# Performance work log

Hardware: AMD Instinct MI355X
Metric: run time of the kernel (lower is better)

## Reference

```python
import jax, jax.numpy as jnp
import numpy as np

D = 256; H = 4; DK = D // H
MAX_ATOMS = 13; EDGE_NUM = 78; PAD = 799; K = 20
PREFIX = MAX_ATOMS * 2 + 2 + EDGE_NUM * 4   # 340, tokens that get positional encoding
SEQ = PREFIX + K                             # 360
NPAIR = EDGE_NUM + MAX_ATOMS                 # 91 atom pairs (i,j), j up to max_atoms
DFF = 2048; MSP = 800; B = 256

# ---- static pair / gather index tables (numpy, computed once) ----
def _pairs():
    pi, pj, pe = [], [], []
    for i in range(MAX_ATOMS):
        base = sum(MAX_ATOMS - jj - 1 for jj in range(i))  # getEdgeIdx prefix
        for j in range(i + 1, MAX_ATOMS + 1):
            pi.append(i); pj.append(j); pe.append(base + (j - i) - 1)
    return np.array(pi), np.array(pj), np.array(pe)

PI, PJ, PEI = _pairs()
_eb = MAX_ATOMS * 2 + 2 + 2 * PEI           # edge feature start in encoder output (stride 2)
GIDX = np.stack([2*PI, 2*PI+1, 2*PJ, 2*PJ+1, _eb, _eb+1, _eb+2, _eb+3], axis=1)  # (91,8)
ZMASK = np.ones((NPAIR, 8), np.float32)
ZMASK[PJ == MAX_ATOMS, 4:] = 0.0            # j == max_atoms -> edge slots zeroed
ES = (MAX_ATOMS + 1) * 2 + 4 * PEI          # edge slice start in raw src (stride 4)
EIDX = ES[:, None] + np.arange(4)[None, :]  # (91,4)

def _pe_table():
    pe = np.zeros((PREFIX, D), np.float32)
    pos = np.arange(PREFIX, dtype=np.float64)[:, None]
    ev = np.arange(0, D, 2)
    pe[:, ev] = np.sin(pos / 10000.0 ** (2 * ev / D))
    pe[:, ev + 1] = np.cos(pos / 10000.0 ** (2 * (ev + 1) / D))
    return jnp.asarray(pe)

PETAB = _pe_table()

def _norm(x, a, b):
    mu = x.mean(-1, keepdims=True)
    sd = x.std(-1, keepdims=True, ddof=1)   # torch std is unbiased
    return a * (x - mu) / (sd + 1e-6) + b

def _out_mask(src):
    # vectorized get_pad_mask10; later conditions override earlier ones
    ai = src[:, 2*PI + 1]; aj = src[:, 2*PJ + 1]
    ti = src[:, 2*PI];     tj = src[:, 2*PJ]
    c1 = (ai == 2) | (aj == 2)                                  # -> [0,0,1]
    c2 = (tj == 1) | (ai == 1) | (aj == 1)                      # -> [0,1,1]
    c3 = (ti == PAD) | (tj == PAD) | (ai == 0) | (aj == 0)      # -> [1,1,1]
    c4 = jnp.asarray(PJ < MAX_ATOMS)[None, :] & jnp.any(src[:, EIDX] == 1, axis=-1)
    m111 = c3 | c4
    return jnp.stack([m111, m111 | c2, m111 | c2 | c1], axis=-1)  # (B,91,3) bool


def setup_inputs() -> dict:
    key = jax.random.key(0)
    ks = jax.random.split(key, 12)
    g = lambda k, shape, s=0.02: jax.random.normal(k, shape, jnp.float32) * s
    emb = g(ks[0], (MSP, D), 1.0).at[PAD].set(0.0)  # nn.Embedding zeroes padding row
    return {
        'src': jax.random.randint(ks[1], (B, SEQ), 0, MSP, dtype=jnp.int32),
        'emb': emb,
        'wq': g(ks[2], (D, D)), 'bq': jnp.zeros((D,), jnp.float32),
        'wk': g(ks[3], (D, D)), 'bk': jnp.zeros((D,), jnp.float32),
        'wv': g(ks[4], (D, D)), 'bv': jnp.zeros((D,), jnp.float32),
        'wo': g(ks[5], (D, D)), 'bo': jnp.zeros((D,), jnp.float32),
        'n1a': jnp.ones((D,), jnp.float32), 'n1b': jnp.zeros((D,), jnp.float32),
        'n2a': jnp.ones((D,), jnp.float32), 'n2b': jnp.zeros((D,), jnp.float32),
        'w1': g(ks[6], (D, DFF)), 'b1': jnp.zeros((DFF,), jnp.float32),
        'w2': g(ks[7], (DFF, D)), 'b2': jnp.zeros((D,), jnp.float32),
        'wl': g(ks[8], (8 * D, 3)), 'bl': jnp.zeros((3,), jnp.float32),
    }


def reference(src, emb, wq, bq, wk, bk, wv, bv, wo, bo, n1a, n1b, n2a, n2b,
              w1, b1, w2, b2, wl, bl):
    Bn, S = src.shape
    x = emb[src]                                             # (B,S,D)
    # positional encoding (scale + PE) only on first PREFIX tokens, dropout=eval/no-op
    xp = x[:, :PREFIX] * jnp.sqrt(jnp.float32(D)) + PETAB
    x = jnp.concatenate([xp, x[:, PREFIX:]], axis=1)
    pad = src != PAD                                         # (B,S) query-row mask
    # encoder layer (pre-norm, residual)
    x2 = _norm(x, n1a, n1b)
    def heads(w, b):
        return (x2 @ w + b).reshape(Bn, S, H, DK).transpose(0, 2, 1, 3)
    q, kk, v = heads(wq, bq), heads(wk, bk), heads(wv, bv)
    sc = jnp.einsum('bhqd,bhkd->bhqk', q, kk) / jnp.sqrt(jnp.float32(DK))
    sc = jnp.where(pad[:, None, :, None], sc, jnp.float32(-1e9))  # mask broadcasts over keys
    ctx = jnp.einsum('bhqk,bhkd->bhqd', jax.nn.softmax(sc, axis=-1), v)
    x = x + ctx.transpose(0, 2, 1, 3).reshape(Bn, S, D) @ wo + bo
    x2 = _norm(x, n2a, n2b)
    x = x + jax.nn.relu(x2 @ w1 + b1) @ w2 + b2
    # triangular atom-pair gather + concat, vectorized via static index table
    feat = x[:, GIDX] * jnp.asarray(ZMASK)[None, :, :, None]  # (B,91,8,D)
    logits = feat.reshape(Bn, NPAIR, 8 * D) @ wl + bl         # (B,91,3)
    return jnp.where(_out_mask(src), jnp.float32(-1e9), logits)
```

## Files before the change

### kernel.cpp

```cpp
#include <hip/hip_runtime.h>
#include <hip/hip_bf16.h>
#include <math.h>


using bf16 = __hip_bfloat16;
typedef __attribute__((ext_vector_type(4))) float f32x4;
typedef __attribute__((ext_vector_type(16))) float f32x16;
typedef long long i64;
typedef unsigned char uchar;

static __device__ __forceinline__ float wave_sum64(float v){
  #pragma unroll
  for (int o = 32; o >= 1; o >>= 1) v += __shfl_xor(v, o, 64);
  return v;
}

static __device__ __forceinline__ void gl_lds16(const void* g, void* l){
  __builtin_amdgcn_global_load_lds((const __attribute__((address_space(1))) void*)g,
                                   (__attribute__((address_space(3))) void*)l, 16, 0, 0);
}

static __device__ __forceinline__ unsigned pack2(float a, float b){
  union { bf16 h[2]; unsigned u; } u;
  u.h[0] = __float2bfloat16(a); u.h[1] = __float2bfloat16(b);
  return u.u;
}

static __device__ __forceinline__ uchar f2f8(float v){
  return (uchar)(__builtin_amdgcn_cvt_pk_fp8_f32(v, 0.f, 0, false) & 0xff);
}
static __device__ __forceinline__ unsigned pack4_fp8(float a, float b, float c, float d){
  int v = __builtin_amdgcn_cvt_pk_fp8_f32(a, b, 0, false);
  v = __builtin_amdgcn_cvt_pk_fp8_f32(c, d, v, true);
  return (unsigned)v;
}

static __device__ __forceinline__ float fexp2(float x){
  float r;
  asm("v_exp_f32 %0, %1" : "=v"(r) : "v"(x));
  return r;
}

__global__ __launch_bounds__(256) void cvt_all(
    const float* s0, const float* s1, const float* s2, const float* s3,
    const float* s4, const float* s5,
    uchar* d0, uchar* d1, uchar* d2, uchar* d3, uchar* d4, uchar* d5)
{
  __shared__ float t[32][33];
  const float* srcs[6] = {s0, s1, s2, s3, s4, s5};
  uchar* dsts[6] = {d0, d1, d2, d3, d4, d5};
  const int Ks[6] = {256, 256, 256, 256, 256, 2048};
  const int Ns[6] = {256, 256, 256, 256, 2048, 256};
  const int offs[7] = {0, 64, 128, 192, 256, 768, 1280};
  int bid = blockIdx.x, j = 5;
  #pragma unroll
  for (int q = 4; q >= 0; q--) if (bid < offs[q + 1]) j = q;
  int local = bid - offs[j];
  int K = Ks[j], N = Ns[j];
  const float* src = srcs[j];
  uchar* dst = dsts[j];
  int kt = K >> 5;
  int kb = (local % kt) * 32, nb = (local / kt) * 32;
  int tx = threadIdx.x & 31, ty = threadIdx.x >> 5;
  #pragma unroll
  for (int dy = 0; dy < 32; dy += 8)
    t[ty + dy][tx] = src[(size_t)(kb + ty + dy) * N + nb + tx];
  __syncthreads();
  #pragma unroll
  for (int dy = 0; dy < 32; dy += 8)
    dst[(size_t)(nb + ty + dy) * K + kb + tx] = f2f8(t[tx][ty + dy]);
}

__global__ __launch_bounds__(256) void embed_ln1(
    const int* __restrict__ src, const float* __restrict__ emb,
    const float* __restrict__ na, const float* __restrict__ nb,
    bf16* __restrict__ x, uchar* __restrict__ xn8)
{
  int row  = blockIdx.x * 4 + (threadIdx.x >> 6);
  int lane = threadIdx.x & 63;
  int s = row % 360;
  int tok = src[row];
  float4 v = *(const float4*)(emb + (size_t)tok * 256 + lane * 4);
  float vv[4] = {v.x, v.y, v.z, v.w};
  if (s < 340){
    const float C = (-2.0f / 256.0f) * 13.287712379549449f;
    #pragma unroll
    for (int t = 0; t < 4; t++){
      int c = lane * 4 + t;
      float ang = (float)s * exp2f(C * (float)c);
      float pe = (c & 1) ? cosf(ang) : sinf(ang);
      vv[t] = 16.0f * vv[t] + pe;
    }
  }
  float sum = wave_sum64(vv[0] + vv[1] + vv[2] + vv[3]);
  float mu = sum * (1.0f / 256.0f);
  float d0 = vv[0]-mu, d1 = vv[1]-mu, d2 = vv[2]-mu, d3 = vv[3]-mu;
  float sq = wave_sum64(d0*d0 + d1*d1 + d2*d2 + d3*d3);
  float inv = 1.0f / (sqrtf(sq * (1.0f / 255.0f)) + 1e-6f);
  bf16 xo[4] = { __float2bfloat16(vv[0]), __float2bfloat16(vv[1]),
                 __float2bfloat16(vv[2]), __float2bfloat16(vv[3]) };
  *(uint2*)(x + (size_t)row * 256 + lane * 4) = *(uint2*)xo;
  float4 a4 = *(const float4*)(na + lane * 4);
  float4 b4 = *(const float4*)(nb + lane * 4);
  unsigned u = pack4_fp8(a4.x * d0 * inv + b4.x, a4.y * d1 * inv + b4.y,
                         a4.z * d2 * inv + b4.z, a4.w * d3 * inv + b4.w);
  *(unsigned*)(xn8 + (size_t)row * 256 + lane * 4) = u;
}

__global__ __launch_bounds__(256) void ln_k8(
    const bf16* __restrict__ x, const float* __restrict__ na,
    const float* __restrict__ nb, uchar* __restrict__ xn8)
{
  int row  = blockIdx.x * 4 + (threadIdx.x >> 6);
  int lane = threadIdx.x & 63;
  uint2 raw = *(const uint2*)(x + (size_t)row * 256 + lane * 4);
  bf16* xr = (bf16*)&raw;
  float v0 = __bfloat162float(xr[0]), v1 = __bfloat162float(xr[1]);
  float v2 = __bfloat162float(xr[2]), v3 = __bfloat162float(xr[3]);
  float sum = wave_sum64(v0 + v1 + v2 + v3);
  float mu = sum * (1.0f / 256.0f);
  float d0 = v0-mu, d1 = v1-mu, d2 = v2-mu, d3 = v3-mu;
  float sq = wave_sum64(d0*d0 + d1*d1 + d2*d2 + d3*d3);
  float inv = 1.0f / (sqrtf(sq * (1.0f / 255.0f)) + 1e-6f);
  float4 a4 = *(const float4*)(na + lane * 4);
  float4 b4 = *(const float4*)(nb + lane * 4);
  unsigned u = pack4_fp8(a4.x * d0 * inv + b4.x, a4.y * d1 * inv + b4.y,
                         a4.z * d2 * inv + b4.z, a4.w * d3 * inv + b4.w);
  *(unsigned*)(xn8 + (size_t)row * 256 + lane * 4) = u;
}

template<int MODE>
__global__ __launch_bounds__(256) void gemm_k256(
    const uchar* __restrict__ A, const uchar* __restrict__ Bt,
    const float* __restrict__ bias,
    uchar* __restrict__ out8, bf16* __restrict__ xres,
    int N, int nTiles,
    const float* __restrict__ bq, const float* __restrict__ bk)
{
  __shared__ __align__(16) char smem[65536];
  uchar* As = (uchar*)smem;
  uchar* Bs = (uchar*)(smem + 32768);
  uchar* S8 = (uchar*)smem;
  bf16 (*Cs)[136] = (bf16 (*)[136])smem;
  int chunk = gridDim.x >> 3;
  int bi = (blockIdx.x & 7) * chunk + (blockIdx.x >> 3);
  int m0 = (bi / nTiles) * 128, n0 = (bi % nTiles) * 128;
  int tid = threadIdx.x;
  int wave = tid >> 6, lane = tid & 63;
  int wm = (wave >> 1) * 64, wn = (wave & 1) * 64;
  int r32 = lane & 31, half = lane >> 5;

  #pragma unroll
  for (int j = 0; j < 8; j++){
    int c = j * 256 + tid;
    int row = c >> 4, p = c & 15;
    int sl = (p & 8) | ((p & 7) ^ (row & 7));
    gl_lds16(A  + (size_t)(m0 + row) * 256 + sl * 16, As + (size_t)c * 16);
    gl_lds16(Bt + (size_t)(n0 + row) * 256 + sl * 16, Bs + (size_t)c * 16);
  }

  f32x16 acc[2][2];
  #pragma unroll
  for (int mb = 0; mb < 2; mb++)
    #pragma unroll
    for (int nb = 0; nb < 2; nb++)
      #pragma unroll
      for (int e = 0; e < 16; e++) acc[mb][nb][e] = 0.f;

  __syncthreads();

  #pragma unroll
  for (int c = 0; c < 8; c++){
    int l0 = 2 * c + half;
    i64 alo[2], ahi[2], blo[2], bhi[2];
    #pragma unroll
    for (int mb = 0; mb < 2; mb++){
      int row = wm + mb * 32 + r32;
      int st = (l0 & 8) | ((l0 & 7) ^ (row & 7));
      uint4 v = *(const uint4*)(As + row * 256 + st * 16);
      alo[mb] = *(const i64*)&v.x;  ahi[mb] = *(const i64*)&v.z;
    }
    #pragma unroll
    for (int nb = 0; nb < 2; nb++){
      int row = wn + nb * 32 + r32;
      int st = (l0 & 8) | ((l0 & 7) ^ (row & 7));
      uint4 v = *(const uint4*)(Bs + row * 256 + st * 16);
      blo[nb] = *(const i64*)&v.x;  bhi[nb] = *(const i64*)&v.z;
    }
    #pragma unroll
    for (int mb = 0; mb < 2; mb++)
      #pragma unroll
      for (int nb = 0; nb < 2; nb++){
        if (MODE == 5){
          acc[mb][nb] = __builtin_amdgcn_mfma_f32_32x32x16_fp8_fp8(alo[mb], blo[nb], acc[mb][nb], 0, 0, 0);
          acc[mb][nb] = __builtin_amdgcn_mfma_f32_32x32x16_fp8_fp8(ahi[mb], bhi[nb], acc[mb][nb], 0, 0, 0);
        } else {
          acc[mb][nb] = __builtin_amdgcn_mfma_f32_32x32x16_fp8_fp8(blo[nb], alo[mb], acc[mb][nb], 0, 0, 0);
          acc[mb][nb] = __builtin_amdgcn_mfma_f32_32x32x16_fp8_fp8(bhi[nb], ahi[mb], acc[mb][nb], 0, 0, 0);
        }
      }
  }

  __syncthreads();

  if (MODE == 4){
    const int region = n0 >> 8;
    const float* bb = (region == 0 ? bq : bk);
    #pragma unroll
    for (int mb = 0; mb < 2; mb++){
      int m_l = wm + mb * 32 + r32;
      #pragma unroll
      for (int nb = 0; nb < 2; nb++)
        #pragma unroll
        for (int g = 0; g < 4; g++){
          int n_l = wn + nb * 32 + g * 8 + half * 4;
          int bidx = (n0 & 255) + n_l;
          float v0 = acc[mb][nb][g * 4 + 0] + bb[bidx + 0];
          float v1 = acc[mb][nb][g * 4 + 1] + bb[bidx + 1];
          float v2 = acc[mb][nb][g * 4 + 2] + bb[bidx + 2];
          float v3 = acc[mb][nb][g * 4 + 3] + bb[bidx + 3];
          *(unsigned*)(S8 + m_l * 136 + n_l) = pack4_fp8(v0, v1, v2, v3);
        }
    }
    __syncthreads();
    int lr = tid >> 1, seg = tid & 1;
    #pragma unroll
    for (int j = 0; j < 4; j++){
      int nl = seg * 64 + j * 16;
      uint2 a = *(uint2*)(S8 + lr * 136 + nl);
      uint2 b = *(uint2*)(S8 + lr * 136 + nl + 8);
      uint4 st = make_uint4(a.x, a.y, b.x, b.y);
      int m = m0 + lr;
      int b_ = m / 360, s = m - b_ * 360;
      int nnl = (n0 & 255) + nl;
      int h = nnl >> 6, dk = nnl & 63;
      size_t roff = (region == 1) ? 23592960ull : 0ull;
      *(uint4*)(out8 + roff + ((size_t)(b_ * 4 + h) * 360 + s) * 64 + dk) = st;
    }
  } else if (MODE == 5){
    #pragma unroll
    for (int nb = 0; nb < 2; nb++){
      int n_l = wn + nb * 32 + r32;
      float bv_ = bias[n0 + n_l];
      #pragma unroll
      for (int mb = 0; mb < 2; mb++)
        #pragma unroll
        for (int g = 0; g < 4; g++){
          int m_l = wm + mb * 32 + g * 8 + half * 4;
          *(unsigned*)(S8 + n_l * 136 + m_l) =
              pack4_fp8(acc[mb][nb][g * 4 + 0] + bv_, acc[mb][nb][g * 4 + 1] + bv_,
                        acc[mb][nb][g * 4 + 2] + bv_, acc[mb][nb][g * 4 + 3] + bv_);
        }
    }
    __syncthreads();
    int nn = tid >> 1, part = tid & 1;
    int nnl = n0 + nn;
    int h = nnl >> 6, dk = nnl & 63;
    #pragma unroll
    for (int j0 = 0; j0 < 64; j0 += 8){
      int mm = m0 + part * 64 + j0;
      int b_ = mm / 360, s = mm - b_ * 360;
      uint2 val = *(uint2*)(S8 + nn * 136 + part * 64 + j0);
      *(uint2*)(out8 + ((size_t)((b_ * 4 + h) * 64 + dk)) * 360 + s) = val;
    }
  } else {
    #pragma unroll
    for (int hb = 0; hb < 2; hb++){
      if ((wave >> 1) == hb){
        #pragma unroll
        for (int mb = 0; mb < 2; mb++){
          int ml = mb * 32 + r32;
          #pragma unroll
          for (int nb = 0; nb < 2; nb++)
            #pragma unroll
            for (int g = 0; g < 4; g++){
              int nl0 = wn + nb * 32 + g * 8 + half * 4;
              float v0 = acc[mb][nb][g * 4 + 0] + bias[n0 + nl0 + 0];
              float v1 = acc[mb][nb][g * 4 + 1] + bias[n0 + nl0 + 1];
              float v2 = acc[mb][nb][g * 4 + 2] + bias[n0 + nl0 + 2];
              float v3 = acc[mb][nb][g * 4 + 3] + bias[n0 + nl0 + 3];
              *(unsigned*)(&Cs[ml][nl0])     = pack2(v0, v1);
              *(unsigned*)(&Cs[ml][nl0 + 2]) = pack2(v2, v3);
            }
        }
      }
      __syncthreads();
      int mbase = m0 + hb * 64;
      int lr = tid >> 2, seg = tid & 3;
      bf16* op = xres + (size_t)(mbase + lr) * 256 + n0 + seg * 32;
      #pragma unroll
      for (int j = 0; j < 4; j++){
        uint4 cv = *(uint4*)(&Cs[lr][seg * 32 + j * 8]);
        uint4 xv = *(uint4*)(op + j * 8);
        bf16* ca = (bf16*)&cv; bf16* xa = (bf16*)&xv;
        bf16 o8[8];
        #pragma unroll
        for (int t = 0; t < 8; t++)
          o8[t] = __float2bfloat16(__bfloat162float(ca[t]) + __bfloat162float(xa[t]));
        *(uint4*)(op + j * 8) = *(uint4*)o8;
      }
      __syncthreads();
    }
  }
}

__global__ __launch_bounds__(512) void gemm_ffn(
    const uchar* __restrict__ A, const uchar* __restrict__ W1t,
    const uchar* __restrict__ W2t, const float* __restrict__ b1,
    const float* __restrict__ b2, bf16* __restrict__ xres)
{
  extern __shared__ __align__(16) char sm[];
  const int W1OFF = 32768, W2OFF = 98304;
  int bi = (blockIdx.x & 7) * 90 + (blockIdx.x >> 3);
  int m0 = bi * 128;
  int tid = threadIdx.x;
  int wave = tid >> 6, lane = tid & 63;
  int wm = (wave & 1) * 64, wn = (wave >> 1) * 64;
  int r32 = lane & 31, half = lane >> 5;

  #pragma unroll
  for (int j = 0; j < 4; j++){
    int c = j * 512 + tid;
    int row = c >> 4, p = c & 15;
    int sl = (p & 8) | ((p & 7) ^ (row & 7));
    gl_lds16(A + (size_t)(m0 + row) * 256 + sl * 16, sm + c * 16);
  }

  f32x16 acc2[2][2];
  #pragma unroll
  for (int mb = 0; mb < 2; mb++)
    #pragma unroll
    for (int nb = 0; nb < 2; nb++)
      #pragma unroll
      for (int e = 0; e < 16; e++) acc2[mb][nb][e] = 0.f;

  for (int s = 0; s < 8; s++){
    #pragma unroll
    for (int j = 0; j < 8; j++){
      int c = j * 512 + tid;
      int row = c >> 4, p = c & 15;
      int sl = (p & 8) | ((p & 7) ^ (row & 7));
      gl_lds16(W1t + (size_t)((s << 8) + row) * 256 + sl * 16, sm + W1OFF + c * 16);
      gl_lds16(W2t + (size_t)row * 2048 + (s << 8) + sl * 16, sm + W2OFF + c * 16);
    }
    __syncthreads();

    f32x16 acc1[2][2];
    #pragma unroll
    for (int mb = 0; mb < 2; mb++)
      #pragma unroll
      for (int nb = 0; nb < 2; nb++)
        #pragma unroll
        for (int e = 0; e < 16; e++) acc1[mb][nb][e] = 0.f;
    #pragma unroll
    for (int c = 0; c < 8; c++){
      int l0 = 2 * c + half;
      i64 alo[2], ahi[2], wlo[2], whi[2];
      #pragma unroll
      for (int mb = 0; mb < 2; mb++){
        int row = wm + mb * 32 + r32;
        int st = (l0 & 8) | ((l0 & 7) ^ (row & 7));
        uint4 v = *(const uint4*)(sm + row * 256 + st * 16);
        alo[mb] = *(const i64*)&v.x;  ahi[mb] = *(const i64*)&v.z;
      }
      #pragma unroll
      for (int nb = 0; nb < 2; nb++){
        int row = wn + nb * 32 + r32;
        int st = (l0 & 8) | ((l0 & 7) ^ (row & 7));
        uint4 v = *(const uint4*)(sm + W1OFF + row * 256 + st * 16);
        wlo[nb] = *(const i64*)&v.x;  whi[nb] = *(const i64*)&v.z;
      }
      #pragma unroll
      for (int mb = 0; mb < 2; mb++)
        #pragma unroll
        for (int nb = 0; nb < 2; nb++){
          acc1[mb][nb] = __builtin_amdgcn_mfma_f32_32x32x16_fp8_fp8(wlo[nb], alo[mb], acc1[mb][nb], 0, 0, 0);
          acc1[mb][nb] = __builtin_amdgcn_mfma_f32_32x32x16_fp8_fp8(whi[nb], ahi[mb], acc1[mb][nb], 0, 0, 0);
        }
    }
    __syncthreads();

    #pragma unroll
    for (int mb = 0; mb < 2; mb++){
      int m = wm + mb * 32 + r32;
      #pragma unroll
      for (int nb = 0; nb < 2; nb++)
        #pragma unroll
        for (int g = 0; g < 4; g++){
          int n_l = wn + nb * 32 + g * 8 + half * 4;
          float4 bv = *(const float4*)(b1 + (s << 8) + n_l);
          float v0 = fmaxf(acc1[mb][nb][g * 4 + 0] + bv.x, 0.f);
          float v1 = fmaxf(acc1[mb][nb][g * 4 + 1] + bv.y, 0.f);
          float v2 = fmaxf(acc1[mb][nb][g * 4 + 2] + bv.z, 0.f);
          float v3 = fmaxf(acc1[mb][nb][g * 4 + 3] + bv.w, 0.f);
          int p_l = n_l >> 4;
          int sl = (p_l & 8) | ((p_l & 7) ^ (m & 7));
          *(unsigned*)(sm + W1OFF + m * 256 + sl * 16 + (n_l & 15)) =
              pack4_fp8(v0, v1, v2, v3);
        }
    }
    __syncthreads();

    #pragma unroll
    for (int c = 0; c < 8; c++){
      int l0 = 2 * c + half;
      i64 hlo[2], hhi[2], wlo[2], whi[2];
      #pragma unroll
      for (int mb = 0; mb < 2; mb++){
        int row = wm + mb * 32 + r32;
        int st = (l0 & 8) | ((l0 & 7) ^ (row & 7));
        uint4 v = *(const uint4*)(sm + W1OFF + row * 256 + st * 16);
        hlo[mb] = *(const i64*)&v.x;  hhi[mb] = *(const i64*)&v.z;
      }
      #pragma unroll
      for (int nb = 0; nb < 2; nb++){
        int row = wn + nb * 32 + r32;
        int st = (l0 & 8) | ((l0 & 7) ^ (row & 7));
        uint4 v = *(const uint4*)(sm + W2OFF + row * 256 + st * 16);
        wlo[nb] = *(const i64*)&v.x;  whi[nb] = *(const i64*)&v.z;
      }
      #pragma unroll
      for (int mb = 0; mb < 2; mb++)
        #pragma unroll
        for (int nb = 0; nb < 2; nb++){
          acc2[mb][nb] = __builtin_amdgcn_mfma_f32_32x32x16_fp8_fp8(wlo[nb], hlo[mb], acc2[mb][nb], 0, 0, 0);
          acc2[mb][nb] = __builtin_amdgcn_mfma_f32_32x32x16_fp8_fp8(whi[nb], hhi[mb], acc2[mb][nb], 0, 0, 0);
        }
    }
    __syncthreads();
  }

  bf16 (*Cs)[136] = (bf16 (*)[136])(sm + W1OFF);
  #pragma unroll
  for (int mb = 0; mb < 2; mb++){
    int ml = wm + mb * 32 + r32;
    #pragma unroll
    for (int nb = 0; nb < 2; nb++)
      #pragma unroll
      for (int g = 0; g < 4; g++){
        int nl0 = wn + nb * 32 + g * 8 + half * 4;
        float4 bv = *(const float4*)(b2 + nl0);
        float v0 = acc2[mb][nb][g * 4 + 0] + bv.x;
        float v1 = acc2[mb][nb][g * 4 + 1] + bv.y;
        float v2 = acc2[mb][nb][g * 4 + 2] + bv.z;
        float v3 = acc2[mb][nb][g * 4 + 3] + bv.w;
        *(unsigned*)(&Cs[ml][nl0])     = pack2(v0, v1);
        *(unsigned*)(&Cs[ml][nl0 + 2]) = pack2(v2, v3);
      }
  }
  __syncthreads();
  int lr = tid >> 2, seg = tid & 3;
  bf16* op = xres + (size_t)(m0 + lr) * 256 + seg * 64;
  #pragma unroll
  for (int j = 0; j < 8; j++){
    uint4 cv = *(uint4*)(&Cs[lr][seg * 64 + j * 8]);
    uint4 xv = *(uint4*)(op + j * 8);
    bf16* ca = (bf16*)&cv; bf16* xa = (bf16*)&xv;
    bf16 o8[8];
    #pragma unroll
    for (int t = 0; t < 8; t++)
      o8[t] = __float2bfloat16(__bfloat162float(ca[t]) + __bfloat162float(xa[t]));
    *(uint4*)(op + j * 8) = *(uint4*)o8;
  }
}

template<bool TAIL>
static __device__ __forceinline__ void attn_step(
    int kc, const uchar (*Ks)[80], uchar (*Pb)[16][48],
    const uchar* __restrict__ vb, int wave, int r, int qd,
    const i64* qa0, const i64* qa1, float* lsum, f32x4 (*accO)[4])
{
  int krow0 = kc * 32 + r;
  int krow1 = krow0 + 16;
  if (TAIL){ if (krow0 > 359) krow0 = 359; if (krow1 > 359) krow1 = 359; }
  i64 kf00 = *(const i64*)(&Ks[krow0][qd * 8]);
  i64 kf01 = *(const i64*)(&Ks[krow0][32 + qd * 8]);
  i64 kf10 = *(const i64*)(&Ks[krow1][qd * 8]);
  i64 kf11 = *(const i64*)(&Ks[krow1][32 + qd * 8]);
  i64 vf[4];
  #pragma unroll
  for (int dt = 0; dt < 4; dt++)
    vf[dt] = *(const i64*)(vb + (size_t)(dt * 16 + r) * 360 + kc * 32 + qd * 8);

  const float CEXP = 0.18033688011112042f;

  #pragma unroll
  for (int tl = 0; tl < 3; tl++){
    f32x4 z0 = {0.f, 0.f, 0.f, 0.f}, z1 = {0.f, 0.f, 0.f, 0.f};
    z0 = __builtin_amdgcn_mfma_f32_16x16x32_fp8_fp8(kf00, qa0[tl], z0, 0, 0, 0);
    z0 = __builtin_amdgcn_mfma_f32_16x16x32_fp8_fp8(kf01, qa1[tl], z0, 0, 0, 0);
    z1 = __builtin_amdgcn_mfma_f32_16x16x32_fp8_fp8(kf10, qa0[tl], z1, 0, 0, 0);
    z1 = __builtin_amdgcn_mfma_f32_16x16x32_fp8_fp8(kf11, qa1[tl], z1, 0, 0, 0);
    float p0[4], p1[4];
    #pragma unroll
    for (int i = 0; i < 4; i++){
      p0[i] = fexp2(z0[i] * CEXP);
      p1[i] = fexp2(z1[i] * CEXP);
      if (TAIL){
        if (kc * 32 + qd * 4 + i >= 360) p0[i] = 0.f;
        if (kc * 32 + 16 + qd * 4 + i >= 360) p1[i] = 0.f;
      }
      lsum[tl] += p0[i] + p1[i];
    }
    *(unsigned*)(&Pb[wave][r][qd * 4])      = pack4_fp8(p0[0], p0[1], p0[2], p0[3]);
    *(unsigned*)(&Pb[wave][r][16 + qd * 4]) = pack4_fp8(p1[0], p1[1], p1[2], p1[3]);
    asm volatile("s_waitcnt lgkmcnt(0)" ::: "memory");
    i64 pa = *(const i64*)(&Pb[wave][r][qd * 8]);
    #pragma unroll
    for (int dt = 0; dt < 4; dt++)
      accO[tl][dt] = __builtin_amdgcn_mfma_f32_16x16x32_fp8_fp8(pa, vf[dt], accO[tl][dt], 0, 0, 0);
    asm volatile("s_waitcnt lgkmcnt(0)" ::: "memory");
  }
}

__global__ __launch_bounds__(512) void attn5(
    const uchar* __restrict__ q, const uchar* __restrict__ kk, const uchar* __restrict__ vt,
    const int* __restrict__ src, uchar* __restrict__ ctx8)
{
  __shared__ __align__(16) uchar smem[34944];
  uchar (*Ks)[80]     = (uchar (*)[80])smem;
  uchar (*Pb)[16][48] = (uchar (*)[16][48])(smem + 28800);
  int bh = blockIdx.x;
  int b = bh >> 2, h = bh & 3;
  int wave = threadIdx.x >> 6, lane = threadIdx.x & 63;
  int r = lane & 15, qd = lane >> 4;
  const uchar* qb = q  + (size_t)bh * 360 * 64;
  const uchar* kb = kk + (size_t)bh * 360 * 64;
  const uchar* vb = vt + (size_t)bh * 64 * 360;
  const int* srow = src + b * 360;

  for (int c = threadIdx.x; c < 1440; c += 512){
    int row = c >> 2, g = c & 3;
    *(uint4*)(&Ks[row][g * 16]) = *(const uint4*)(kb + row * 64 + g * 16);
  }
  __syncthreads();

  i64 qa0[3], qa1[3];
  float lsum[3];
  f32x4 accO[3][4];
  #pragma unroll
  for (int tl = 0; tl < 3; tl++){
    int qt = wave * 3 + tl;
    int qg = qt * 16 + r;
    int qrow = qg > 359 ? 359 : qg;
    bool qp = (qg < 360) && (srow[qg] == 799);
    i64 a0 = *(const i64*)(qb + qrow * 64 + qd * 8);
    i64 a1 = *(const i64*)(qb + qrow * 64 + 32 + qd * 8);
    qa0[tl] = qp ? 0 : a0;
    qa1[tl] = qp ? 0 : a1;
    lsum[tl] = 0.f;
    #pragma unroll
    for (int dt = 0; dt < 4; dt++) accO[tl][dt] = (f32x4){0.f, 0.f, 0.f, 0.f};
  }

  for (int kc = 0; kc < 11; kc++)
    attn_step<false>(kc, Ks, Pb, vb, wave, r, qd, qa0, qa1, lsum, accO);
  attn_step<true>(11, Ks, Pb, vb, wave, r, qd, qa0, qa1, lsum, accO);

  __syncthreads();
  uchar* Cw = smem + wave * 1280;

  #pragma unroll
  for (int tl = 0; tl < 3; tl++){
    float ls = lsum[tl];
    ls += __shfl_xor(ls, 16, 64);
    ls += __shfl_xor(ls, 32, 64);
    float invl = 1.0f / ls;
    #pragma unroll
    for (int dt = 0; dt < 4; dt++)
      *(unsigned*)(Cw + r * 80 + dt * 16 + qd * 4) =
          pack4_fp8(accO[tl][dt][0] * invl, accO[tl][dt][1] * invl,
                    accO[tl][dt][2] * invl, accO[tl][dt][3] * invl);
    asm volatile("s_waitcnt lgkmcnt(0)" ::: "memory");
    int qt = wave * 3 + tl;
    int qglob = qt * 16 + r;
    if (qglob < 360)
      *(uint4*)(ctx8 + ((size_t)(b * 360 + qglob)) * 256 + h * 64 + qd * 16) =
          *(uint4*)(Cw + r * 80 + qd * 16);
    asm volatile("s_waitcnt lgkmcnt(0)" ::: "memory");
  }
}

__global__ __launch_bounds__(256) void head_k(
    const bf16* __restrict__ x, const int* __restrict__ src,
    const float* __restrict__ wl, const float* __restrict__ bl,
    float* __restrict__ out)
{
  __shared__ bf16 Xs[192][264];
  int b = blockIdx.x;
  int tid = threadIdx.x;
  int wave = tid >> 6, lane = tid & 63;
  int g = lane >> 3, sub = lane & 7;

  const bf16* xb = x + (size_t)b * 360 * 256;
  for (int it = 0; it < 24; it++){
    int idx = tid + it * 256;
    int row = idx >> 5, col = idx & 31;
    *(uint4*)(&Xs[row][col * 8]) = *(const uint4*)(xb + row * 256 + col * 8);
  }

  float wv[96];
  {
    const float4* wr4 = (const float4*)(wl + (size_t)(g * 256 + sub * 32) * 3);
    #pragma unroll
    for (int c = 0; c < 24; c++) *(float4*)(&wv[c * 4]) = wr4[c];
  }
  float bl0 = bl[0], bl1 = bl[1], bl2 = bl[2];
  const int* sr = src + b * 360;
  __syncthreads();

  for (int p = wave; p < 91; p += 4){
    int i = 0, rem = p;
    while (rem >= 13 - i){ rem -= 13 - i; i++; }
    int j = i + 1 + rem;
    int base = 12 * i - (i * (i - 1)) / 2;
    int pe = base + (j - i) - 1;
    int eb = 28 + 2 * pe;

    int idxg;
    if (g == 0) idxg = 2 * i;
    else if (g == 1) idxg = 2 * i + 1;
    else if (g == 2) idxg = 2 * j;
    else if (g == 3) idxg = 2 * j + 1;
    else idxg = eb + (g - 4);
    bool zm = !(g >= 4 && j == 13);

    uint4 xv[4];
    #pragma unroll
    for (int c = 0; c < 4; c++) xv[c] = *(uint4*)(&Xs[idxg][sub * 32 + c * 8]);
    const bf16* xa = (const bf16*)xv;
    float a0 = 0.f, a1 = 0.f, a2 = 0.f;
    #pragma unroll
    for (int t = 0; t < 32; t++){
      float f = zm ? __bfloat162float(xa[t]) : 0.0f;
      a0 += f * wv[t * 3 + 0];
      a1 += f * wv[t * 3 + 1];
      a2 += f * wv[t * 3 + 2];
    }
    #pragma unroll
    for (int o = 1; o < 64; o <<= 1){
      a0 += __shfl_xor(a0, o, 64);
      a1 += __shfl_xor(a1, o, 64);
      a2 += __shfl_xor(a2, o, 64);
    }
    if (lane == 0){
      int ti = sr[2 * i], ai = sr[2 * i + 1], tj = sr[2 * j], aj = sr[2 * j + 1];
      bool c1 = (ai == 2) || (aj == 2);
      bool c2 = (tj == 1) || (ai == 1) || (aj == 1);
      bool c3 = (ti == 799) || (tj == 799) || (ai == 0) || (aj == 0);
      bool c4 = false;
      if (j < 13){
        int es = 28 + 4 * pe;
        c4 = (sr[es] == 1) || (sr[es + 1] == 1) || (sr[es + 2] == 1) || (sr[es + 3] == 1);
      }
      bool m1 = c3 || c4, m2 = m1 || c2, m3 = m2 || c1;
      float* op = out + ((size_t)b * 91 + p) * 3;
      op[0] = m1 ? -1.0e9f : (a0 + bl0);
      op[1] = m2 ? -1.0e9f : (a1 + bl1);
      op[2] = m3 ? -1.0e9f : (a2 + bl2);
    }
  }
}

extern "C" void kernel_launch(void* const* d_in, const int* in_sizes, int n_in,
                              void* d_out, int out_size, void* d_ws, size_t ws_size,
                              hipStream_t stream)
{
  const int*   src = (const int*)  d_in[0];
  const float* emb = (const float*)d_in[1];
  const float* wq  = (const float*)d_in[2];  const float* bq = (const float*)d_in[3];
  const float* wk  = (const float*)d_in[4];  const float* bk = (const float*)d_in[5];
  const float* wv  = (const float*)d_in[6];  const float* bv = (const float*)d_in[7];
  const float* wo  = (const float*)d_in[8];  const float* bo = (const float*)d_in[9];
  const float* n1a = (const float*)d_in[10]; const float* n1b = (const float*)d_in[11];
  const float* n2a = (const float*)d_in[12]; const float* n2b = (const float*)d_in[13];
  const float* w1  = (const float*)d_in[14]; const float* b1 = (const float*)d_in[15];
  const float* w2  = (const float*)d_in[16]; const float* b2 = (const float*)d_in[17];
  const float* wl  = (const float*)d_in[18]; const float* bl = (const float*)d_in[19];
  float* out = (float*)d_out;

  if (ws_size < 191365120ull) return;

  char* ws = (char*)d_ws;
  bf16*  x    = (bf16*)(ws);
  uchar* xn8  = (uchar*)(ws + 47185920ull);
  char*  R    = ws + 70778880ull;
  uchar* q8   = (uchar*)(R);
  uchar* vt8  = (uchar*)(R + 47185920ull);
  char*  wC   = ws + 165150720ull;
  uchar* wqkv8 = (uchar*)(wC);
  uchar* wo8   = (uchar*)(wC + 196608);
  uchar* w1f8T = (uchar*)(wC + 262144);
  uchar* w2f8T = (uchar*)(wC + 786432);

  cvt_all<<<1280, 256, 0, stream>>>(wq, wk, wv, wo, w1, w2,
                                    wqkv8, wqkv8 + 65536, wqkv8 + 131072,
                                    wo8, w1f8T, w2f8T);

  embed_ln1<<<23040, 256, 0, stream>>>(src, emb, n1a, n1b, x, xn8);

  gemm_k256<4><<<2880, 256, 0, stream>>>(xn8, wqkv8, nullptr, q8, nullptr,
                                         512, 4, bq, bk);
  gemm_k256<5><<<1440, 256, 0, stream>>>(xn8, wqkv8 + 131072, bv, vt8, nullptr,
                                         256, 2, nullptr, nullptr);

  attn5<<<1024, 512, 0, stream>>>(q8, q8 + 23592960ull, vt8, src, xn8 );

  gemm_k256<3><<<1440, 256, 0, stream>>>(xn8, wo8, bo, nullptr, x,
                                         256, 2, nullptr, nullptr);

  ln_k8<<<23040, 256, 0, stream>>>(x, n2a, n2b, xn8);

  gemm_ffn<<<720, 512, 163840, stream>>>(xn8, w1f8T, w2f8T, b1, b2, x);

  head_k<<<256, 256, 0, stream>>>(x, src, wl, bl, out);
}
```

Before: 533.1 us.

## Double-buffer FFN weight chunks in LDS with half-width hidden slices

The fused FFN kernel now walks the hidden dimension in 16 chunks of 128 instead of 8 chunks of 256. W1/W2 tiles are double-buffered in LDS, so the next chunk's global-to-LDS loads are issued while the current chunk's ReLU epilogue and second GEMM run. The goal is to hide weight-load latency that the old load-then-sync loop exposed at every step. In exchange there are twice as many loop iterations and barriers, a narrower first-GEMM tile per wave, and a custom barrier that waits only on lgkmcnt, whose correctness for the global_load_lds buffers depends on the later __syncthreads.

```diff
diff --git a/kernel.cpp b/kernel.cpp
--- a/kernel.cpp
+++ b/kernel.cpp
@@ -18,6 +18,11 @@
 static __device__ __forceinline__ void gl_lds16(const void* g, void* l){
   __builtin_amdgcn_global_load_lds((const __attribute__((address_space(1))) void*)g,
                                    (__attribute__((address_space(3))) void*)l, 16, 0, 0);
+}
+
+static __device__ __forceinline__ void barrier_lgkm(){
+  asm volatile("s_waitcnt lgkmcnt(0)" ::: "memory");
+  __builtin_amdgcn_s_barrier();
 }
 
 static __device__ __forceinline__ unsigned pack2(float a, float b){
@@ -316,6 +321,7 @@
   int tid = threadIdx.x;
   int wave = tid >> 6, lane = tid & 63;
   int wm = (wave & 1) * 64, wn = (wave >> 1) * 64;
+  int wnh = (wave >> 1) * 32;
   int r32 = lane & 31, half = lane >> 5;
 
   #pragma unroll
@@ -325,6 +331,16 @@
     int sl = (p & 8) | ((p & 7) ^ (row & 7));
     gl_lds16(A + (size_t)(m0 + row) * 256 + sl * 16, sm + c * 16);
   }
+  #pragma unroll
+  for (int j = 0; j < 4; j++){
+    int c = j * 512 + tid;
+    int row1 = c >> 4, p1 = c & 15;
+    int sl1 = (p1 & 8) | ((p1 & 7) ^ (row1 & 7));
+    gl_lds16(W1t + (size_t)row1 * 256 + sl1 * 16, sm + W1OFF + c * 16);
+    int row2 = c >> 3, p2 = c & 7;
+    int sl2 = p2 ^ (row2 & 7);
+    gl_lds16(W2t + (size_t)row2 * 2048 + sl2 * 16, sm + W2OFF + c * 16);
+  }
 
   f32x16 acc2[2][2];
   #pragma unroll
@@ -334,28 +350,22 @@
       #pragma unroll
       for (int e = 0; e < 16; e++) acc2[mb][nb][e] = 0.f;
 
-  for (int s = 0; s < 8; s++){
-    #pragma unroll
-    for (int j = 0; j < 8; j++){
-      int c = j * 512 + tid;
-      int row = c >> 4, p = c & 15;
-      int sl = (p & 8) | ((p & 7) ^ (row & 7));
-      gl_lds16(W1t + (size_t)((s << 8) + row) * 256 + sl * 16, sm + W1OFF + c * 16);
-      gl_lds16(W2t + (size_t)row * 2048 + (s << 8) + sl * 16, sm + W2OFF + c * 16);
-    }
-    __syncthreads();
-
-    f32x16 acc1[2][2];
+  __syncthreads();
+
+  int cur = 0;
+  for (int s = 0; s < 16; s++){
+    const int w1o = W1OFF + cur * 32768;
+    const int w2o = W2OFF + cur * 32768;
+
+    f32x16 acc1[2];
     #pragma unroll
     for (int mb = 0; mb < 2; mb++)
       #pragma unroll
-      for (int nb = 0; nb < 2; nb++)
-        #pragma unroll
-        for (int e = 0; e < 16; e++) acc1[mb][nb][e] = 0.f;
+      for (int e = 0; e < 16; e++) acc1[mb][e] = 0.f;
     #pragma unroll
     for (int c = 0; c < 8; c++){
       int l0 = 2 * c + half;
-      i64 alo[2], ahi[2], wlo[2], whi[2];
+      i64 alo[2], ahi[2];
       #pragma unroll
       for (int mb = 0; mb < 2; mb++){
         int row = wm + mb * 32 + r32;
@@ -363,60 +373,68 @@
         uint4 v = *(const uint4*)(sm + row * 256 + st * 16);
         alo[mb] = *(const i64*)&v.x;  ahi[mb] = *(const i64*)&v.z;
       }
+      int roww = wnh + r32;
+      int stw = (l0 & 8) | ((l0 & 7) ^ (roww & 7));
+      uint4 w = *(const uint4*)(sm + w1o + roww * 256 + stw * 16);
+      i64 wlo = *(const i64*)&w.x, whi = *(const i64*)&w.z;
+      #pragma unroll
+      for (int mb = 0; mb < 2; mb++){
+        acc1[mb] = __builtin_amdgcn_mfma_f32_32x32x16_fp8_fp8(wlo, alo[mb], acc1[mb], 0, 0, 0);
+        acc1[mb] = __builtin_amdgcn_mfma_f32_32x32x16_fp8_fp8(whi, ahi[mb], acc1[mb], 0, 0, 0);
+      }
+    }
+    barrier_lgkm();
+
+    if (s < 15){
+      int nxt = cur ^ 1;
+      #pragma unroll
+      for (int j = 0; j < 4; j++){
+        int c = j * 512 + tid;
+        int row1 = c >> 4, p1 = c & 15;
+        int sl1 = (p1 & 8) | ((p1 & 7) ^ (row1 & 7));
+        gl_lds16(W1t + (size_t)((s + 1) * 128 + row1) * 256 + sl1 * 16,
+                 sm + W1OFF + nxt * 32768 + c * 16);
+        int row2 = c >> 3, p2 = c & 7;
+        int sl2 = p2 ^ (row2 & 7);
+        gl_lds16(W2t + (size_t)row2 * 2048 + (s + 1) * 128 + sl2 * 16,
+                 sm + W2OFF + nxt * 32768 + c * 16);
+      }
+    }
+
+    #pragma unroll
+    for (int mb = 0; mb < 2; mb++){
+      int m = wm + mb * 32 + r32;
+      #pragma unroll
+      for (int g = 0; g < 4; g++){
+        int n_l = wnh + g * 8 + half * 4;
+        float4 bv = *(const float4*)(b1 + s * 128 + n_l);
+        float v0 = fmaxf(acc1[mb][g * 4 + 0] + bv.x, 0.f);
+        float v1 = fmaxf(acc1[mb][g * 4 + 1] + bv.y, 0.f);
+        float v2 = fmaxf(acc1[mb][g * 4 + 2] + bv.z, 0.f);
+        float v3 = fmaxf(acc1[mb][g * 4 + 3] + bv.w, 0.f);
+        int sl = (n_l >> 4) ^ (m & 7);
+        *(unsigned*)(sm + w1o + m * 128 + sl * 16 + (n_l & 15)) =
+            pack4_fp8(v0, v1, v2, v3);
+      }
+    }
+    barrier_lgkm();
+
+    #pragma unroll
+    for (int c = 0; c < 4; c++){
+      int l0 = 2 * c + half;
+      i64 hlo[2], hhi[2], wlo[2], whi[2];
+      #pragma unroll
+      for (int mb = 0; mb < 2; mb++){
+        int row = wm + mb * 32 + r32;
+        int st = l0 ^ (row & 7);
+        uint4 v = *(const uint4*)(sm + w1o + row * 128 + st * 16);
+        hlo[mb] = *(const i64*)&v.x;  hhi[mb] = *(const i64*)&v.z;
+      }
       #pragma unroll
       for (int nb = 0; nb < 2; nb++){
         int row = wn + nb * 32 + r32;
-        int st = (l0 & 8) | ((l0 & 7) ^ (row & 7));
-        uint4 v = *(const uint4*)(sm + W1OFF + row * 256 + st * 16);
-        wlo[nb] = *(const i64*)&v.x;  whi[nb] = *(const i64*)&v.z;
-      }
-      #pragma unroll
-      for (int mb = 0; mb < 2; mb++)
-        #pragma unroll
-        for (int nb = 0; nb < 2; nb++){
-          acc1[mb][nb] = __builtin_amdgcn_mfma_f32_32x32x16_fp8_fp8(wlo[nb], alo[mb], acc1[mb][nb], 0, 0, 0);
-          acc1[mb][nb] = __builtin_amdgcn_mfma_f32_32x32x16_fp8_fp8(whi[nb], ahi[mb], acc1[mb][nb], 0, 0, 0);
-        }
-    }
-    __syncthreads();
-
-    #pragma unroll
-    for (int mb = 0; mb < 2; mb++){
-      int m = wm + mb * 32 + r32;
-      #pragma unroll
-      for (int nb = 0; nb < 2; nb++)
-        #pragma unroll
-        for (int g = 0; g < 4; g++){
-          int n_l = wn + nb * 32 + g * 8 + half * 4;
-          float4 bv = *(const float4*)(b1 + (s << 8) + n_l);
-          float v0 = fmaxf(acc1[mb][nb][g * 4 + 0] + bv.x, 0.f);
-          float v1 = fmaxf(acc1[mb][nb][g * 4 + 1] + bv.y, 0.f);
-          float v2 = fmaxf(acc1[mb][nb][g * 4 + 2] + bv.z, 0.f);
-          float v3 = fmaxf(acc1[mb][nb][g * 4 + 3] + bv.w, 0.f);
-          int p_l = n_l >> 4;
-          int sl = (p_l & 8) | ((p_l & 7) ^ (m & 7));
-          *(unsigned*)(sm + W1OFF + m * 256 + sl * 16 + (n_l & 15)) =
-              pack4_fp8(v0, v1, v2, v3);
-        }
-    }
-    __syncthreads();
-
-    #pragma unroll
-    for (int c = 0; c < 8; c++){
-      int l0 = 2 * c + half;
-      i64 hlo[2], hhi[2], wlo[2], whi[2];
-      #pragma unroll
-      for (int mb = 0; mb < 2; mb++){
-        int row = wm + mb * 32 + r32;
-        int st = (l0 & 8) | ((l0 & 7) ^ (row & 7));
-        uint4 v = *(const uint4*)(sm + W1OFF + row * 256 + st * 16);
-        hlo[mb] = *(const i64*)&v.x;  hhi[mb] = *(const i64*)&v.z;
-      }
-      #pragma unroll
-      for (int nb = 0; nb < 2; nb++){
-        int row = wn + nb * 32 + r32;
-        int st = (l0 & 8) | ((l0 & 7) ^ (row & 7));
-        uint4 v = *(const uint4*)(sm + W2OFF + row * 256 + st * 16);
+        int st = l0 ^ (row & 7);
+        uint4 v = *(const uint4*)(sm + w2o + row * 128 + st * 16);
         wlo[nb] = *(const i64*)&v.x;  whi[nb] = *(const i64*)&v.z;
       }
       #pragma unroll
@@ -428,6 +446,7 @@
         }
     }
     __syncthreads();
+    cur ^= 1;
   }
 
   bf16 (*Cs)[136] = (bf16 (*)[136])(sm + W1OFF);
```

Result: faster. 510.9 us (-4.2%).
